# Optimization experiments

Measured on AMD Instinct MI355X. Metric: run time of the kernel, lower is better.

Reference implementation:

```python
import jax, jax.numpy as jnp
import numpy as np

HIDDEN = 128
EDGE_DIM = 32
N_NODES = 50000
N_EDGES = 800000


def setup_inputs() -> dict:
    key = jax.random.key(0)
    ks = jax.random.split(key, 8)
    node_features = jax.random.normal(ks[0], (N_NODES, HIDDEN), dtype=jnp.float32)
    edge_index = jax.random.randint(ks[1], (2, N_EDGES), 0, N_NODES, dtype=jnp.int64)
    edge_attr = jax.random.normal(ks[2], (N_EDGES, EDGE_DIM), dtype=jnp.float32)
    # parameters (Linear stored as [in, out] for x @ W + b)
    s_et = 1.0 / np.sqrt(EDGE_DIM)
    W_edge = jax.random.uniform(ks[3], (EDGE_DIM, HIDDEN), jnp.float32, -s_et, s_et)
    b_edge = jnp.zeros((HIDDEN,), jnp.float32)
    s1 = 1.0 / np.sqrt(3 * HIDDEN)
    W1 = jax.random.uniform(ks[4], (3 * HIDDEN, HIDDEN), jnp.float32, -s1, s1)
    b1 = jnp.zeros((HIDDEN,), jnp.float32)
    s2 = 1.0 / np.sqrt(HIDDEN)
    W2 = jax.random.uniform(ks[5], (HIDDEN, 1), jnp.float32, -s2, s2)
    b2 = jnp.zeros((1,), jnp.float32)
    return {
        "node_features": node_features,
        "edge_attr": edge_attr,
        "W_edge": W_edge, "b_edge": b_edge,
        "W1": W1, "b1": b1, "W2": W2, "b2": b2,
        "edge_index": edge_index,
    }


def reference(node_features, edge_attr, W_edge, b_edge, W1, b1, W2, b2, edge_index):
    row, col = edge_index[0], edge_index[1]
    src = node_features[row]                 # [E, H] gather
    dst = node_features[col]                 # [E, H] gather
    edge_feat = edge_attr @ W_edge + b_edge  # [E, H]
    combined = jnp.concatenate([src, edge_feat, dst], axis=-1)  # [E, 3H]
    h = jax.nn.relu(combined @ W1 + b1)      # [E, H]
    attn = jax.nn.sigmoid(h @ W2 + b2)       # [E, 1]
    return attn
```

## Files before the change

### kernel.cpp

```cpp
#include <hip/hip_runtime.h>
#include <hip/hip_bf16.h>

#define HIDDEN   128
#define EDGE_DIM 32
#define NNODE    50000
#define NEDGE    800000
#define KSTEPS   9
#define NFRAG    8
#define LDS_KS   8

typedef __attribute__((ext_vector_type(4))) float        f32x4;
typedef __attribute__((ext_vector_type(8))) short        bf16x8;
typedef __attribute__((ext_vector_type(4))) unsigned int u32x4;

#define BPACK_USHORTS  (KSTEPS * NFRAG * 64 * 8)
#define BIAS_OFF_BYTES (BPACK_USHORTS * 2)
#define FLAG_OFF_BYTES (BIAS_OFF_BYTES + 128 * 4)
#define NODE_OFF_BYTES 74752
#define IDX_OFF_BYTES  (NODE_OFF_BYTES + NNODE * HIDDEN * 2)
#define WS_NEEDED      (IDX_OFF_BYTES + 2 * NEDGE * 4)

__device__ __forceinline__ unsigned short f2bf(float f) {
  unsigned u = __builtin_bit_cast(unsigned, f);
  u += 0x7FFFu + ((u >> 16) & 1u);
  return (unsigned short)(u >> 16);
}

__device__ __forceinline__ unsigned cvt_pk_bf16(float a, float b) {
  union { __hip_bfloat162 h; unsigned u; } cv;
  cv.h = __float22bfloat162_rn(make_float2(a, b));
  return cv.u;
}

__device__ __forceinline__ bf16x8 pack8(f32x4 lo, f32x4 hi) {
  u32x4 u;
  u[0] = cvt_pk_bf16(lo[0], lo[1]);
  u[1] = cvt_pk_bf16(lo[2], lo[3]);
  u[2] = cvt_pk_bf16(hi[0], hi[1]);
  u[3] = cvt_pk_bf16(hi[2], hi[3]);
  return __builtin_bit_cast(bf16x8, u);
}

__device__ __forceinline__ void gload_lds16(const void* g, void* l) {
  __builtin_amdgcn_global_load_lds(
      (const __attribute__((address_space(1))) unsigned int*)g,
      (__attribute__((address_space(3))) unsigned int*)l, 16, 0, 0);
}

#define MFMA(a, b, c) __builtin_amdgcn_mfma_f32_16x16x32_bf16((a), (b), (c), 0, 0, 0)

__global__ void setup_kernel(const float* __restrict__ W_edge,
                             const float* __restrict__ b_edge,
                             const float* __restrict__ W1,
                             const float* __restrict__ b1,
                             const void*  __restrict__ eidx,
                             unsigned short* __restrict__ Bpack,
                             float* __restrict__ bias_eff,
                             int*   __restrict__ flag64) {
  const int bid = blockIdx.x, tid = threadIdx.x;
  if (bid < 36) {
    const int pair  = bid * 2 + (tid >> 6);
    const int lane  = tid & 63;
    const int kstep = pair >> 3;
    const int f     = pair & 7;
    const int col   = f * 16 + (lane & 15);
    const int kbase = kstep * 32 + (lane >> 4) * 8;
    float vals[8];
#pragma unroll
    for (int j = 0; j < 8; ++j) {
      const int k = kbase + j;
      float val;
      if (k < 128) {
        val = W1[k * 128 + col];
      } else if (k < 256) {
        val = W1[(k + 128) * 128 + col];
      } else {
        const int kk = k - 256;
        float s = 0.f;
        for (int t = 0; t < 128; ++t)
          s = fmaf(W_edge[kk * 128 + t], W1[(128 + t) * 128 + col], s);
        val = s;
      }
      vals[j] = val;
    }
    u32x4 sv;
#pragma unroll
    for (int j = 0; j < 4; ++j)
      sv[j] = (unsigned)f2bf(vals[2 * j]) | ((unsigned)f2bf(vals[2 * j + 1]) << 16);
    *(u32x4*)(Bpack + ((kstep * NFRAG + f) * 64 + lane) * 8) = sv;
  } else {
    if (tid < 128) {
      float s = b1[tid];
      for (int t = 0; t < 128; ++t)
        s = fmaf(b_edge[t], W1[(128 + t) * 128 + tid], s);
      bias_eff[tid] = s;
    }
    if (tid == 0) {
      const unsigned* w = (const unsigned*)eidx;
      int all0 = 1;
      for (int i = 0; i < 64; ++i) all0 &= (w[2 * i + 1] == 0u) ? 1 : 0;
      *flag64 = all0;
    }
  }
}

__global__ __launch_bounds__(256) void cvt_nodes_kernel(const float* __restrict__ nodef,
                                                        unsigned short* __restrict__ nbf) {
  const int i = blockIdx.x * 256 + threadIdx.x;
  if (i >= NNODE * HIDDEN / 8) return;
  f32x4 lo = *(const f32x4*)(nodef + i * 8);
  f32x4 hi = *(const f32x4*)(nodef + i * 8 + 4);
  *(bf16x8*)(nbf + i * 8) = pack8(lo, hi);
}

__global__ __launch_bounds__(256) void cvt_idx_kernel(const void* __restrict__ eidx,
                                                      const int* __restrict__ flag64,
                                                      int* __restrict__ idx32) {
  const int i = blockIdx.x * 256 + threadIdx.x;
  if (i >= 2 * NEDGE) return;
  if (*flag64) idx32[i] = (int)((const long long*)eidx)[i];
  else         idx32[i] = ((const int*)eidx)[i];
}

__global__ __launch_bounds__(512, 4) void edge_attn_kernel(
    const unsigned short* __restrict__ nbf,
    const float* __restrict__ eattr,
    const int*   __restrict__ idx32,
    const unsigned short* __restrict__ Bpack,
    const float* __restrict__ bias_eff,
    const float* __restrict__ W2,
    const float* __restrict__ b2,
    float* __restrict__ out) {
  __shared__ unsigned short lds_b[LDS_KS * NFRAG * 64 * 8];

  const int tid   = threadIdx.x;
  const int lane  = tid & 63;
  const int wid   = tid >> 6;
  const int l15   = lane & 15;
  const int kg    = lane >> 4;
  const int ebase = blockIdx.x * 256 + wid * 32;

#pragma unroll
  for (int i = 0; i < 8; ++i) {
    const char* g = (const char*)Bpack + (size_t)(i * 512 + tid) * 16;
    char*       l = (char*)lds_b + (size_t)(i * 512 + wid * 64) * 16;
    gload_lds16(g, l);
  }

  const int r0 = idx32[ebase + l15];
  const int r1 = idx32[ebase + 16 + l15];
  const int c0 = idx32[NEDGE + ebase + l15];
  const int c1 = idx32[NEDGE + ebase + 16 + l15];

  bf16x8 a0[4], a1[4];
#pragma unroll
  for (int ks = 0; ks < 4; ++ks) {
    a0[ks] = *(const bf16x8*)(nbf + (size_t)r0 * HIDDEN + kg * 8 + ks * 32);
    a1[ks] = *(const bf16x8*)(nbf + (size_t)r1 * HIDDEN + kg * 8 + ks * 32);
  }

  __syncthreads();

  f32x4 acc[2][NFRAG];
#pragma unroll
  for (int m = 0; m < 2; ++m)
#pragma unroll
    for (int f = 0; f < NFRAG; ++f)
      acc[m][f] = (f32x4){0.f, 0.f, 0.f, 0.f};

#pragma unroll
  for (int ks = 0; ks < 4; ++ks)
#pragma unroll
    for (int f = 0; f < NFRAG; ++f) {
      bf16x8 bfr = *(const bf16x8*)(lds_b + ((ks * NFRAG + f) * 64 + lane) * 8);
      acc[0][f] = MFMA(a0[ks], bfr, acc[0][f]);
      acc[1][f] = MFMA(a1[ks], bfr, acc[1][f]);
    }

  __builtin_amdgcn_sched_barrier(0);

#pragma unroll
  for (int ks = 0; ks < 4; ++ks) {
    a0[ks] = *(const bf16x8*)(nbf + (size_t)c0 * HIDDEN + kg * 8 + ks * 32);
    a1[ks] = *(const bf16x8*)(nbf + (size_t)c1 * HIDDEN + kg * 8 + ks * 32);
  }

#pragma unroll
  for (int ks = 0; ks < 4; ++ks)
#pragma unroll
    for (int f = 0; f < NFRAG; ++f) {
      bf16x8 bfr = *(const bf16x8*)(lds_b + (((ks + 4) * NFRAG + f) * 64 + lane) * 8);
      acc[0][f] = MFMA(a0[ks], bfr, acc[0][f]);
      acc[1][f] = MFMA(a1[ks], bfr, acc[1][f]);
    }

  __builtin_amdgcn_sched_barrier(0);

  bf16x8 ae0, ae1;
  {
    const float* pe = eattr + (size_t)(ebase + l15) * EDGE_DIM + kg * 8;
    f32x4 lo = *(const f32x4*)(pe);
    f32x4 hi = *(const f32x4*)(pe + 4);
    ae0 = pack8(lo, hi);
  }
  {
    const float* pe = eattr + (size_t)(ebase + 16 + l15) * EDGE_DIM + kg * 8;
    f32x4 lo = *(const f32x4*)(pe);
    f32x4 hi = *(const f32x4*)(pe + 4);
    ae1 = pack8(lo, hi);
  }
#pragma unroll
  for (int f = 0; f < NFRAG; ++f) {
    bf16x8 bfr = *(const bf16x8*)(Bpack + ((8 * NFRAG + f) * 64 + lane) * 8);
    acc[0][f] = MFMA(ae0, bfr, acc[0][f]);
    acc[1][f] = MFMA(ae1, bfr, acc[1][f]);
  }

  float w2v[NFRAG], bv[NFRAG];
#pragma unroll
  for (int f = 0; f < NFRAG; ++f) {
    w2v[f] = W2[f * 16 + l15];
    bv[f]  = bias_eff[f * 16 + l15];
  }
  const float bias2 = b2[0];

  float part[2][4];
#pragma unroll
  for (int m = 0; m < 2; ++m)
#pragma unroll
    for (int rr = 0; rr < 4; ++rr) {
      float s = 0.f;
#pragma unroll
      for (int f = 0; f < NFRAG; ++f) {
        float h = fmaxf(acc[m][f][rr] + bv[f], 0.f);
        s = fmaf(h, w2v[f], s);
      }
      part[m][rr] = s;
    }

#pragma unroll
  for (int mask = 1; mask < 16; mask <<= 1)
#pragma unroll
    for (int m = 0; m < 2; ++m)
#pragma unroll
      for (int rr = 0; rr < 4; ++rr)
        part[m][rr] += __shfl_xor(part[m][rr], mask, 64);

  if (l15 == 0) {
#pragma unroll
    for (int m = 0; m < 2; ++m)
#pragma unroll
      for (int rr = 0; rr < 4; ++rr) {
        float x = part[m][rr] + bias2;
        out[ebase + m * 16 + kg * 4 + rr] = 1.f / (1.f + __expf(-x));
      }
  }
}

__global__ __launch_bounds__(256) void edge_attn_kernel_fp32(
    const float* __restrict__ nodef,
    const float* __restrict__ eattr,
    const void*  __restrict__ eidx,
    const unsigned short* __restrict__ Bpack,
    const float* __restrict__ bias_eff,
    const float* __restrict__ W2,
    const float* __restrict__ b2,
    const int*   __restrict__ flag64,
    float* __restrict__ out) {
  const int lane  = threadIdx.x & 63;
  const int wid   = threadIdx.x >> 6;
  const int ebase = blockIdx.x * 128 + wid * 32;
  const int l15   = lane & 15;
  const int kg    = lane >> 4;
  const int koff  = kg * 8;
  const int e0 = ebase + l15;
  const int e1 = e0 + 16;

  long r0, c0, r1, c1;
  if (*flag64) {
    const long long* p = (const long long*)eidx;
    r0 = (long)p[e0];          r1 = (long)p[e1];
    c0 = (long)p[NEDGE + e0];  c1 = (long)p[NEDGE + e1];
  } else {
    const int* p = (const int*)eidx;
    r0 = p[e0];          r1 = p[e1];
    c0 = p[NEDGE + e0];  c1 = p[NEDGE + e1];
  }

  f32x4 acc[2][NFRAG];
#pragma unroll
  for (int m = 0; m < 2; ++m)
#pragma unroll
    for (int f = 0; f < NFRAG; ++f)
      acc[m][f] = (f32x4){0.f, 0.f, 0.f, 0.f};

#pragma unroll 1
  for (int ks = 0; ks < KSTEPS; ++ks) {
    const float *p0, *p1;
    if (ks < 4)      { p0 = nodef + r0 * HIDDEN + ks * 32;       p1 = nodef + r1 * HIDDEN + ks * 32; }
    else if (ks < 8) { p0 = nodef + c0 * HIDDEN + (ks - 4) * 32; p1 = nodef + c1 * HIDDEN + (ks - 4) * 32; }
    else             { p0 = eattr + (long)e0 * EDGE_DIM;         p1 = eattr + (long)e1 * EDGE_DIM; }

    f32x4 lo0 = *(const f32x4*)(p0 + koff);
    f32x4 hi0 = *(const f32x4*)(p0 + koff + 4);
    f32x4 lo1 = *(const f32x4*)(p1 + koff);
    f32x4 hi1 = *(const f32x4*)(p1 + koff + 4);
    bf16x8 a0 = pack8(lo0, hi0);
    bf16x8 a1 = pack8(lo1, hi1);

#pragma unroll
    for (int f = 0; f < NFRAG; ++f) {
      bf16x8 bfr = *(const bf16x8*)(Bpack + ((ks * NFRAG + f) * 64 + lane) * 8);
      acc[0][f] = MFMA(a0, bfr, acc[0][f]);
      acc[1][f] = MFMA(a1, bfr, acc[1][f]);
    }
  }

  float w2v[NFRAG], bv[NFRAG];
#pragma unroll
  for (int f = 0; f < NFRAG; ++f) {
    w2v[f] = W2[f * 16 + l15];
    bv[f]  = bias_eff[f * 16 + l15];
  }
  const float bias2 = b2[0];

  float part[2][4];
#pragma unroll
  for (int m = 0; m < 2; ++m)
#pragma unroll
    for (int r = 0; r < 4; ++r) {
      float s = 0.f;
#pragma unroll
      for (int f = 0; f < NFRAG; ++f) {
        float h = acc[m][f][r] + bv[f];
        h = fmaxf(h, 0.f);
        s = fmaf(h, w2v[f], s);
      }
      part[m][r] = s;
    }

#pragma unroll
  for (int mask = 1; mask < 16; mask <<= 1)
#pragma unroll
    for (int m = 0; m < 2; ++m)
#pragma unroll
      for (int r = 0; r < 4; ++r)
        part[m][r] += __shfl_xor(part[m][r], mask, 64);

  if (l15 == 0) {
#pragma unroll
    for (int m = 0; m < 2; ++m)
#pragma unroll
      for (int r = 0; r < 4; ++r) {
        float x = part[m][r] + bias2;
        out[ebase + m * 16 + kg * 4 + r] = 1.f / (1.f + __expf(-x));
      }
  }
}

extern "C" void kernel_launch(void* const* d_in, const int* in_sizes, int n_in,
                              void* d_out, int out_size, void* d_ws, size_t ws_size,
                              hipStream_t stream) {
  const float* nodef  = (const float*)d_in[0];
  const float* eattr  = (const float*)d_in[1];
  const float* W_edge = (const float*)d_in[2];
  const float* b_edge = (const float*)d_in[3];
  const float* W1     = (const float*)d_in[4];
  const float* b1     = (const float*)d_in[5];
  const float* W2     = (const float*)d_in[6];
  const float* b2     = (const float*)d_in[7];
  const void*  eidx   = d_in[8];

  unsigned short* Bpack    = (unsigned short*)d_ws;
  float*          bias_eff = (float*)((char*)d_ws + BIAS_OFF_BYTES);
  int*            flag64   = (int*)((char*)d_ws + FLAG_OFF_BYTES);
  unsigned short* nbf      = (unsigned short*)((char*)d_ws + NODE_OFF_BYTES);
  int*            idx32    = (int*)((char*)d_ws + IDX_OFF_BYTES);

  setup_kernel<<<dim3(37), dim3(128), 0, stream>>>(W_edge, b_edge, W1, b1, eidx,
                                                   Bpack, bias_eff, flag64);

  if (ws_size >= (size_t)WS_NEEDED) {
    cvt_idx_kernel<<<dim3((2 * NEDGE + 255) / 256), dim3(256), 0, stream>>>(eidx, flag64, idx32);
    cvt_nodes_kernel<<<dim3((NNODE * HIDDEN / 8 + 255) / 256), dim3(256), 0, stream>>>(nodef, nbf);
    edge_attn_kernel<<<dim3(NEDGE / 256), dim3(512), 0, stream>>>(
        nbf, eattr, idx32, Bpack, bias_eff, W2, b2, (float*)d_out);
  } else {
    edge_attn_kernel_fp32<<<dim3(NEDGE / 128), dim3(256), 0, stream>>>(
        nodef, eattr, eidx, Bpack, bias_eff, W2, b2, flag64, (float*)d_out);
  }
}
```

Before: 128.8 us.

## Precompute per-node projections P and Q before edge gather

Splits the first linear layer algebraically so that node_features @ W1_src (plus bias) and node_features @ W1_dst are computed once per node in a new pq_kernel and stored as bf16. The edge kernel then gathers the projected P[row] and Q[col] rows, adds them to the small edge_attr matmul, and applies ReLU, the W2 dot product and the sigmoid. This removes the per-edge 256-wide K matmul, cutting MFMA work per edge by a large factor while keeping the gather volume the same. It needs more workspace for two projected tables, and the projections are now rounded to bf16 after the matmul rather than before.

New measurement: 112.9 us. 12.3% less time.

```diff
diff --git a/kernel.cpp b/kernel.cpp
--- a/kernel.cpp
+++ b/kernel.cpp
@@ -16,9 +16,16 @@
 #define BPACK_USHORTS  (KSTEPS * NFRAG * 64 * 8)
 #define BIAS_OFF_BYTES (BPACK_USHORTS * 2)
 #define FLAG_OFF_BYTES (BIAS_OFF_BYTES + 128 * 4)
-#define NODE_OFF_BYTES 74752
+#define DATA_OFF       74752
+
+#define PP_OFF   DATA_OFF
+#define QP_OFF   (PP_OFF + NNODE * HIDDEN * 2)
+#define IDXN_OFF (QP_OFF + NNODE * HIDDEN * 2)
+#define WS_NEW   (IDXN_OFF + 2 * NEDGE * 4)
+
+#define NODE_OFF_BYTES DATA_OFF
 #define IDX_OFF_BYTES  (NODE_OFF_BYTES + NNODE * HIDDEN * 2)
-#define WS_NEEDED      (IDX_OFF_BYTES + 2 * NEDGE * 4)
+#define WS_R8          (IDX_OFF_BYTES + 2 * NEDGE * 4)
 
 __device__ __forceinline__ unsigned short f2bf(float f) {
   unsigned u = __builtin_bit_cast(unsigned, f);
@@ -122,6 +129,209 @@
   else         idx32[i] = ((const int*)eidx)[i];
 }
 
+__global__ __launch_bounds__(512, 2) void pq_kernel(
+    const float* __restrict__ nodef,
+    const unsigned short* __restrict__ Bpack,
+    const float* __restrict__ bias_eff,
+    unsigned* __restrict__ Pp,
+    unsigned* __restrict__ Qp) {
+  __shared__ unsigned short lds_b[LDS_KS * NFRAG * 64 * 8];
+
+  const int tid  = threadIdx.x;
+  const int lane = tid & 63;
+  const int wid  = tid >> 6;
+  const int l15  = lane & 15;
+  const int kg   = lane >> 4;
+  const int nb   = blockIdx.x * 256 + wid * 32;
+
+#pragma unroll
+  for (int i = 0; i < 8; ++i) {
+    const char* g = (const char*)Bpack + (size_t)(i * 512 + tid) * 16;
+    char*       l = (char*)lds_b + (size_t)(i * 512 + wid * 64) * 16;
+    gload_lds16(g, l);
+  }
+
+  const int n0 = min(nb + l15, NNODE - 1);
+  const int n1 = min(nb + 16 + l15, NNODE - 1);
+  bf16x8 a0[4], a1[4];
+#pragma unroll
+  for (int ks = 0; ks < 4; ++ks) {
+    const float* p0 = nodef + (size_t)n0 * HIDDEN + ks * 32 + kg * 8;
+    const float* p1 = nodef + (size_t)n1 * HIDDEN + ks * 32 + kg * 8;
+    a0[ks] = pack8(*(const f32x4*)p0, *(const f32x4*)(p0 + 4));
+    a1[ks] = pack8(*(const f32x4*)p1, *(const f32x4*)(p1 + 4));
+  }
+
+  float bv[NFRAG];
+#pragma unroll
+  for (int f = 0; f < NFRAG; ++f) bv[f] = bias_eff[f * 16 + l15];
+
+  __syncthreads();
+
+  f32x4 acc[2][NFRAG];
+#pragma unroll
+  for (int m = 0; m < 2; ++m)
+#pragma unroll
+    for (int f = 0; f < NFRAG; ++f)
+      acc[m][f] = (f32x4){bv[f], bv[f], bv[f], bv[f]};
+#pragma unroll
+  for (int ks = 0; ks < 4; ++ks)
+#pragma unroll
+    for (int f = 0; f < NFRAG; ++f) {
+      bf16x8 bfr = *(const bf16x8*)(lds_b + ((ks * NFRAG + f) * 64 + lane) * 8);
+      acc[0][f] = MFMA(a0[ks], bfr, acc[0][f]);
+      acc[1][f] = MFMA(a1[ks], bfr, acc[1][f]);
+    }
+#pragma unroll
+  for (int m = 0; m < 2; ++m)
+#pragma unroll
+    for (int r = 0; r < 4; ++r) {
+      const int n = nb + m * 16 + kg * 4 + r;
+      if (n < NNODE) {
+#pragma unroll
+        for (int k = 0; k < 4; ++k)
+          Pp[(size_t)n * 64 + k * 16 + l15] =
+              cvt_pk_bf16(acc[m][2 * k][r], acc[m][2 * k + 1][r]);
+      }
+    }
+
+#pragma unroll
+  for (int m = 0; m < 2; ++m)
+#pragma unroll
+    for (int f = 0; f < NFRAG; ++f)
+      acc[m][f] = (f32x4){0.f, 0.f, 0.f, 0.f};
+#pragma unroll
+  for (int ks = 0; ks < 4; ++ks)
+#pragma unroll
+    for (int f = 0; f < NFRAG; ++f) {
+      bf16x8 bfr = *(const bf16x8*)(lds_b + (((ks + 4) * NFRAG + f) * 64 + lane) * 8);
+      acc[0][f] = MFMA(a0[ks], bfr, acc[0][f]);
+      acc[1][f] = MFMA(a1[ks], bfr, acc[1][f]);
+    }
+#pragma unroll
+  for (int m = 0; m < 2; ++m)
+#pragma unroll
+    for (int r = 0; r < 4; ++r) {
+      const int n = nb + m * 16 + kg * 4 + r;
+      if (n < NNODE) {
+#pragma unroll
+        for (int k = 0; k < 4; ++k)
+          Qp[(size_t)n * 64 + k * 16 + l15] =
+              cvt_pk_bf16(acc[m][2 * k][r], acc[m][2 * k + 1][r]);
+      }
+    }
+}
+
+__global__ __launch_bounds__(256, 3) void edge_attn_pq(
+    const float* __restrict__ eattr,
+    const int*   __restrict__ idx32,
+    const unsigned* __restrict__ Pp,
+    const unsigned* __restrict__ Qp,
+    const unsigned short* __restrict__ Bpack,
+    const float* __restrict__ W2,
+    const float* __restrict__ b2,
+    float* __restrict__ out) {
+  const int tid   = threadIdx.x;
+  const int lane  = tid & 63;
+  const int wid   = tid >> 6;
+  const int l15   = lane & 15;
+  const int kg    = lane >> 4;
+  const int ebase = blockIdx.x * 128 + wid * 32;
+
+  const f32x4 zero4 = {0.f, 0.f, 0.f, 0.f};
+
+  int rn[2][4], cn[2][4];
+#pragma unroll
+  for (int m = 0; m < 2; ++m)
+#pragma unroll
+    for (int r = 0; r < 4; ++r) {
+      rn[m][r] = idx32[ebase + m * 16 + kg * 4 + r];
+      cn[m][r] = idx32[NEDGE + ebase + m * 16 + kg * 4 + r];
+    }
+
+  bf16x8 ae0, ae1;
+  {
+    const float* pe = eattr + (size_t)(ebase + l15) * EDGE_DIM + kg * 8;
+    ae0 = pack8(*(const f32x4*)pe, *(const f32x4*)(pe + 4));
+  }
+  {
+    const float* pe = eattr + (size_t)(ebase + 16 + l15) * EDGE_DIM + kg * 8;
+    ae1 = pack8(*(const f32x4*)pe, *(const f32x4*)(pe + 4));
+  }
+
+  f32x4 acc[2][NFRAG];
+#pragma unroll
+  for (int f = 0; f < NFRAG; ++f) {
+    bf16x8 bfr = *(const bf16x8*)(Bpack + ((8 * NFRAG + f) * 64 + lane) * 8);
+    acc[0][f] = MFMA(ae0, bfr, zero4);
+    acc[1][f] = MFMA(ae1, bfr, zero4);
+  }
+
+  unsigned pu[2][4][4], qu[2][4][4];
+#pragma unroll
+  for (int m = 0; m < 2; ++m)
+#pragma unroll
+    for (int r = 0; r < 4; ++r) {
+      const unsigned* pb = Pp + (size_t)rn[m][r] * 64 + l15;
+      const unsigned* qb = Qp + (size_t)cn[m][r] * 64 + l15;
+#pragma unroll
+      for (int k = 0; k < 4; ++k) {
+        pu[m][r][k] = pb[k * 16];
+        qu[m][r][k] = qb[k * 16];
+      }
+    }
+
+#pragma unroll
+  for (int m = 0; m < 2; ++m)
+#pragma unroll
+    for (int r = 0; r < 4; ++r)
+#pragma unroll
+      for (int k = 0; k < 4; ++k) {
+        const unsigned up = pu[m][r][k], uq = qu[m][r][k];
+        acc[m][2 * k][r]     += __builtin_bit_cast(float, up << 16)
+                              + __builtin_bit_cast(float, uq << 16);
+        acc[m][2 * k + 1][r] += __builtin_bit_cast(float, up & 0xffff0000u)
+                              + __builtin_bit_cast(float, uq & 0xffff0000u);
+      }
+
+  float w2v[NFRAG];
+#pragma unroll
+  for (int f = 0; f < NFRAG; ++f) w2v[f] = W2[f * 16 + l15];
+  const float bias2 = b2[0];
+
+  float part[2][4];
+#pragma unroll
+  for (int m = 0; m < 2; ++m)
+#pragma unroll
+    for (int rr = 0; rr < 4; ++rr) {
+      float s = 0.f;
+#pragma unroll
+      for (int f = 0; f < NFRAG; ++f) {
+        float h = fmaxf(acc[m][f][rr], 0.f);
+        s = fmaf(h, w2v[f], s);
+      }
+      part[m][rr] = s;
+    }
+
+#pragma unroll
+  for (int mask = 1; mask < 16; mask <<= 1)
+#pragma unroll
+    for (int m = 0; m < 2; ++m)
+#pragma unroll
+      for (int rr = 0; rr < 4; ++rr)
+        part[m][rr] += __shfl_xor(part[m][rr], mask, 64);
+
+  if (l15 == 0) {
+#pragma unroll
+    for (int m = 0; m < 2; ++m)
+#pragma unroll
+      for (int rr = 0; rr < 4; ++rr) {
+        float x = part[m][rr] + bias2;
+        out[ebase + m * 16 + kg * 4 + rr] = 1.f / (1.f + __expf(-x));
+      }
+  }
+}
+
 __global__ __launch_bounds__(512, 4) void edge_attn_kernel(
     const unsigned short* __restrict__ nbf,
     const float* __restrict__ eattr,
@@ -199,15 +409,11 @@
   bf16x8 ae0, ae1;
   {
     const float* pe = eattr + (size_t)(ebase + l15) * EDGE_DIM + kg * 8;
-    f32x4 lo = *(const f32x4*)(pe);
-    f32x4 hi = *(const f32x4*)(pe + 4);
-    ae0 = pack8(lo, hi);
+    ae0 = pack8(*(const f32x4*)pe, *(const f32x4*)(pe + 4));
   }
   {
     const float* pe = eattr + (size_t)(ebase + 16 + l15) * EDGE_DIM + kg * 8;
-    f32x4 lo = *(const f32x4*)(pe);
-    f32x4 hi = *(const f32x4*)(pe + 4);
-    ae1 = pack8(lo, hi);
+    ae1 = pack8(*(const f32x4*)pe, *(const f32x4*)(pe + 4));
   }
 #pragma unroll
   for (int f = 0; f < NFRAG; ++f) {
@@ -374,13 +580,21 @@
   unsigned short* Bpack    = (unsigned short*)d_ws;
   float*          bias_eff = (float*)((char*)d_ws + BIAS_OFF_BYTES);
   int*            flag64   = (int*)((char*)d_ws + FLAG_OFF_BYTES);
-  unsigned short* nbf      = (unsigned short*)((char*)d_ws + NODE_OFF_BYTES);
-  int*            idx32    = (int*)((char*)d_ws + IDX_OFF_BYTES);
 
   setup_kernel<<<dim3(37), dim3(128), 0, stream>>>(W_edge, b_edge, W1, b1, eidx,
                                                    Bpack, bias_eff, flag64);
 
-  if (ws_size >= (size_t)WS_NEEDED) {
+  if (ws_size >= (size_t)WS_NEW) {
+    unsigned* Pp    = (unsigned*)((char*)d_ws + PP_OFF);
+    unsigned* Qp    = (unsigned*)((char*)d_ws + QP_OFF);
+    int*      idx32 = (int*)((char*)d_ws + IDXN_OFF);
+    cvt_idx_kernel<<<dim3((2 * NEDGE + 255) / 256), dim3(256), 0, stream>>>(eidx, flag64, idx32);
+    pq_kernel<<<dim3((NNODE + 255) / 256), dim3(512), 0, stream>>>(nodef, Bpack, bias_eff, Pp, Qp);
+    edge_attn_pq<<<dim3(NEDGE / 128), dim3(256), 0, stream>>>(
+        eattr, idx32, Pp, Qp, Bpack, W2, b2, (float*)d_out);
+  } else if (ws_size >= (size_t)WS_R8) {
+    unsigned short* nbf   = (unsigned short*)((char*)d_ws + NODE_OFF_BYTES);
+    int*            idx32 = (int*)((char*)d_ws + IDX_OFF_BYTES);
     cvt_idx_kernel<<<dim3((2 * NEDGE + 255) / 256), dim3(256), 0, stream>>>(eidx, flag64, idx32);
     cvt_nodes_kernel<<<dim3((NNODE * HIDDEN / 8 + 255) / 256), dim3(256), 0, stream>>>(nodef, nbf);
     edge_attn_kernel<<<dim3(NEDGE / 256), dim3(512), 0, stream>>>(
```
